# Kernel tuning notes

Hardware: AMD Instinct MI355X
Metric: run time of the kernel (lower is better)

Reference implementation:

```python
import jax, jax.numpy as jnp
import numpy as np
from jax import lax

INSZ, HSZ, NLAYERS = 1024, 1024, 2
B, T = 32, 512
FORGET_BIAS = 1.0


def setup_inputs() -> dict:
    key = jax.random.key(0)
    ks = jax.random.split(key, 6)
    x = jax.random.normal(ks[0], (B, T, INSZ), dtype=jnp.float32)
    lengths = jax.random.randint(ks[1], (B,), 1, T + 1, dtype=jnp.int32)
    s0 = 1.0 / np.sqrt(INSZ + HSZ)
    s1 = 1.0 / np.sqrt(HSZ + HSZ)
    W0 = jax.random.uniform(ks[2], (INSZ + HSZ, 4 * HSZ), jnp.float32, -s0, s0)
    b0 = jnp.zeros((4 * HSZ,), jnp.float32)
    W1 = jax.random.uniform(ks[3], (HSZ + HSZ, 4 * HSZ), jnp.float32, -s1, s1)
    b1 = jnp.zeros((4 * HSZ,), jnp.float32)
    return {"x": x, "lengths": lengths, "W0": W0, "b0": b0, "W1": W1, "b1": b1}


def _lstm_layer(x, lengths, W, b):
    # x: [B, T, D_in]; TF LSTMCell gate order (i, j, f, o), forget_bias added to f.
    bsz = x.shape[0]
    hsz = b.shape[0] // 4
    tsteps = jnp.arange(x.shape[1])

    def step(carry, inp):
        h, c = carry
        xt, t = inp
        z = jnp.concatenate([xt, h], axis=-1) @ W + b  # [B, 4H]
        i, j, f, o = jnp.split(z, 4, axis=-1)
        c_new = jax.nn.sigmoid(f + FORGET_BIAS) * c + jax.nn.sigmoid(i) * jnp.tanh(j)
        h_new = jax.nn.sigmoid(o) * jnp.tanh(c_new)
        mask = (t < lengths)[:, None]
        # dynamic_rnn: zero outputs past sequence_length, freeze state
        h_out = jnp.where(mask, h_new, 0.0)
        h_keep = jnp.where(mask, h_new, h)
        c_keep = jnp.where(mask, c_new, c)
        return (h_keep, c_keep), h_out

    init = (jnp.zeros((bsz, hsz), x.dtype), jnp.zeros((bsz, hsz), x.dtype))
    (h_fin, c_fin), ys = lax.scan(step, init, (jnp.swapaxes(x, 0, 1), tsteps))
    return jnp.swapaxes(ys, 0, 1), h_fin, c_fin


def reference(x, lengths, W0, b0, W1, b1):
    out0, _, _ = _lstm_layer(x, lengths, W0, b0)
    out1, h1, c1 = _lstm_layer(out0, lengths, W1, b1)
    return out1, (h1, c1)
```

## Files before the change

kernel.cpp:

```cpp
#include <hip/hip_runtime.h>
#include <hip/hip_bf16.h>

typedef unsigned short u16;
typedef unsigned int u32;
typedef unsigned long long u64;
typedef short s8v __attribute__((ext_vector_type(8)));
typedef float f4v __attribute__((ext_vector_type(4)));

#define BQ 32
#define TQ 512
#define DQ 1024
#define CHUNK 128
#define NCHUNK (TQ / CHUNK)
#define NTHR 256
#define NBLK_R 256
#define NGRP 16
#define NSUB (NBLK_R / NGRP)

__device__ __host__ inline u16 f2bf(float f) {
    union { float f; unsigned u; } v; v.f = f;
    unsigned r = v.u + 0x7fffu + ((v.u >> 16) & 1u);
    return (u16)(r >> 16);
}
__device__ __host__ inline float bf2f(u16 u) {
    union { unsigned u; float f; } v; v.u = ((unsigned)u) << 16;
    return v.f;
}

__global__ void init_kernel(u32* __restrict__ zero32, size_t nzero) {
    size_t i = (size_t)blockIdx.x * blockDim.x + threadIdx.x;
    size_t stride = (size_t)gridDim.x * blockDim.x;
    for (size_t idx = i; idx < nzero; idx += stride) zero32[idx] = 0;
}

__device__ inline void unpack_pk(uint4 A, uint4 B, s8v& hi, s8v& lo) {
    union { u32 u[4]; s8v v; } H, L;
    H.u[0] = (A.x >> 16) | (A.y & 0xffff0000u); L.u[0] = (A.x & 0xffffu) | (A.y << 16);
    H.u[1] = (A.z >> 16) | (A.w & 0xffff0000u); L.u[1] = (A.z & 0xffffu) | (A.w << 16);
    H.u[2] = (B.x >> 16) | (B.y & 0xffff0000u); L.u[2] = (B.x & 0xffffu) | (B.y << 16);
    H.u[3] = (B.z >> 16) | (B.w & 0xffff0000u); L.u[3] = (B.z & 0xffffu) | (B.w << 16);
    hi = H.v; lo = L.v;
}

__global__ __launch_bounds__(NTHR) void xproj_gemm_kernel(
    const float* __restrict__ in_f32,
    const u32* __restrict__ in_pk,
    const float* __restrict__ W,
    const float* __restrict__ bias,
    float* __restrict__ zx,
    int t0)
{
    __shared__ u16 As[2][128][40];
    __shared__ u16 Bs[2][128][40];

    const int tid = threadIdx.x;
    const int bm = blockIdx.x & 31;
    const int bn = blockIdx.x >> 5;

    const int wv = tid >> 6;
    const int wm = wv >> 1, wn = wv & 1;
    const int lane = tid & 63;
    const int frow = lane & 15;
    const int quad = lane >> 4;

    const int am = tid >> 1;
    const int akh = (tid & 1) * 16;
    const int amg = bm * 128 + am;
    const int ab = amg >> 7;
    const int atl = amg & 127;
    const size_t arow = ((size_t)ab * TQ + t0 + atl) * DQ;

    const int bk = tid >> 3;
    const int bng = (tid & 7) * 16;

    f4v acc[4][4];
    #pragma unroll
    for (int i = 0; i < 4; ++i)
        #pragma unroll
        for (int j = 0; j < 4; ++j) acc[i][j] = (f4v){0.f, 0.f, 0.f, 0.f};

    for (int kt = 0; kt < 32; ++kt) {
        const int k0 = kt * 32;
        if (in_f32) {
            const float* src = in_f32 + arow + k0 + akh;
            #pragma unroll
            for (int j4 = 0; j4 < 4; ++j4) {
                float4 v = ((const float4*)src)[j4];
                float vv[4] = {v.x, v.y, v.z, v.w};
                #pragma unroll
                for (int e = 0; e < 4; ++e) {
                    u16 hh = f2bf(vv[e]);
                    As[0][am][akh + j4 * 4 + e] = hh;
                    As[1][am][akh + j4 * 4 + e] = f2bf(vv[e] - bf2f(hh));
                }
            }
        } else {
            const u32* src = in_pk + arow + k0 + akh;
            #pragma unroll
            for (int j4 = 0; j4 < 4; ++j4) {
                uint4 v = ((const uint4*)src)[j4];
                u32 vv[4] = {v.x, v.y, v.z, v.w};
                #pragma unroll
                for (int e = 0; e < 4; ++e) {
                    As[0][am][akh + j4 * 4 + e] = (u16)(vv[e] >> 16);
                    As[1][am][akh + j4 * 4 + e] = (u16)(vv[e] & 0xffffu);
                }
            }
        }
        {
            const float* wsrc = W + (size_t)(k0 + bk) * (4 * DQ) + bn * 128 + bng;
            #pragma unroll
            for (int j4 = 0; j4 < 4; ++j4) {
                float4 v = ((const float4*)wsrc)[j4];
                float vv[4] = {v.x, v.y, v.z, v.w};
                #pragma unroll
                for (int e = 0; e < 4; ++e) {
                    u16 hh = f2bf(vv[e]);
                    int n = bng + j4 * 4 + e;
                    Bs[0][n][bk] = hh;
                    Bs[1][n][bk] = f2bf(vv[e] - bf2f(hh));
                }
            }
        }
        __syncthreads();

        s8v ah[4], al[4], bh[4], bl[4];
        #pragma unroll
        for (int mt = 0; mt < 4; ++mt) {
            ah[mt] = *(const s8v*)&As[0][wm * 64 + mt * 16 + frow][quad * 8];
            al[mt] = *(const s8v*)&As[1][wm * 64 + mt * 16 + frow][quad * 8];
        }
        #pragma unroll
        for (int nt = 0; nt < 4; ++nt) {
            bh[nt] = *(const s8v*)&Bs[0][wn * 64 + nt * 16 + frow][quad * 8];
            bl[nt] = *(const s8v*)&Bs[1][wn * 64 + nt * 16 + frow][quad * 8];
        }
        #pragma unroll
        for (int mt = 0; mt < 4; ++mt)
            #pragma unroll
            for (int nt = 0; nt < 4; ++nt) {
                acc[mt][nt] = __builtin_amdgcn_mfma_f32_16x16x32_bf16(ah[mt], bh[nt], acc[mt][nt], 0, 0, 0);
                acc[mt][nt] = __builtin_amdgcn_mfma_f32_16x16x32_bf16(al[mt], bh[nt], acc[mt][nt], 0, 0, 0);
                acc[mt][nt] = __builtin_amdgcn_mfma_f32_16x16x32_bf16(ah[mt], bl[nt], acc[mt][nt], 0, 0, 0);
            }
        __syncthreads();
    }

    float bv[4];
    #pragma unroll
    for (int nt = 0; nt < 4; ++nt) bv[nt] = bias[bn * 128 + wn * 64 + nt * 16 + frow];
    #pragma unroll
    for (int mt = 0; mt < 4; ++mt) {
        #pragma unroll
        for (int nt = 0; nt < 4; ++nt) {
            int col = bn * 128 + wn * 64 + nt * 16 + frow;
            #pragma unroll
            for (int r = 0; r < 4; ++r) {
                int row = bm * 128 + wm * 64 + mt * 16 + quad * 4 + r;
                zx[(size_t)row * (4 * DQ) + col] = acc[mt][nt][r] + bv[nt];
            }
        }
    }
}

__global__ __launch_bounds__(NTHR, 1) void lstm_rec_kernel(
    const float* __restrict__ zx,
    const float* __restrict__ W,
    const int* __restrict__ lens,
    u32* __restrict__ h32,
    u32* __restrict__ subc,
    u32* __restrict__ topc,
    float* __restrict__ state_h,
    float* __restrict__ state_c,
    u32* __restrict__ out_pk,
    float* __restrict__ out_f32,
    float* __restrict__ hc_out,
    int t0, int is_last)
{
    __shared__ u16 wt[2][32][1032];
    __shared__ float red[4][16][36];

    const int tid = threadIdx.x;
    const int blk = blockIdx.x;
    const int bg = blk & 1;
    const int cg = blk >> 1;
    const int grp = blk & (NGRP - 1);

    for (int idx = tid; idx < 32 * 1024; idx += NTHR) {
        int n = idx & 31, k = idx >> 5;
        int c = n >> 2, g = n & 3;
        float w = W[(size_t)(DQ + k) * (4 * DQ) + g * DQ + cg * 8 + c];
        u16 wh = f2bf(w);
        wt[0][n][k] = wh;
        wt[1][n][k] = f2bf(w - bf2f(wh));
    }

    const int gb_l = tid >> 3;
    const int gc = tid & 7;
    const int b_g = bg * 16 + gb_l;
    const int hcol = cg * 8 + gc;
    float c_state = 0.f, h_state = 0.f;
    int mylen = 0;
    if (tid < 128) {
        mylen = lens[b_g];
        h_state = state_h[(size_t)b_g * DQ + hcol];
        c_state = state_c[(size_t)b_g * DQ + hcol];
    }

    const int wave = tid >> 6;
    const int lane = tid & 63;
    const int frow = lane & 15;
    const int quad = lane >> 4;
    const int ksrc = wave * 256;
    const u32* hrow = h32 + (size_t)(bg * 16 + frow) * DQ + ksrc + quad * 8;

    __syncthreads();

    const int tend = t0 + CHUNK;
    for (int t = t0; t < tend; ++t) {
        const u32* hp = hrow + (size_t)((t & 1) ^ 1) * (BQ * DQ);
        uint4 q[16];
        asm volatile(
            "global_load_dwordx4 %0, %16, off sc0 sc1\n\t"
            "global_load_dwordx4 %1, %16, off offset:16 sc0 sc1\n\t"
            "global_load_dwordx4 %2, %16, off offset:128 sc0 sc1\n\t"
            "global_load_dwordx4 %3, %16, off offset:144 sc0 sc1\n\t"
            "global_load_dwordx4 %4, %16, off offset:256 sc0 sc1\n\t"
            "global_load_dwordx4 %5, %16, off offset:272 sc0 sc1\n\t"
            "global_load_dwordx4 %6, %16, off offset:384 sc0 sc1\n\t"
            "global_load_dwordx4 %7, %16, off offset:400 sc0 sc1\n\t"
            "global_load_dwordx4 %8, %16, off offset:512 sc0 sc1\n\t"
            "global_load_dwordx4 %9, %16, off offset:528 sc0 sc1\n\t"
            "global_load_dwordx4 %10, %16, off offset:640 sc0 sc1\n\t"
            "global_load_dwordx4 %11, %16, off offset:656 sc0 sc1\n\t"
            "global_load_dwordx4 %12, %16, off offset:768 sc0 sc1\n\t"
            "global_load_dwordx4 %13, %16, off offset:784 sc0 sc1\n\t"
            "global_load_dwordx4 %14, %16, off offset:896 sc0 sc1\n\t"
            "global_load_dwordx4 %15, %16, off offset:912 sc0 sc1\n\t"
            "s_waitcnt vmcnt(0)"
            : "=&v"(q[0]), "=&v"(q[1]), "=&v"(q[2]), "=&v"(q[3]),
              "=&v"(q[4]), "=&v"(q[5]), "=&v"(q[6]), "=&v"(q[7]),
              "=&v"(q[8]), "=&v"(q[9]), "=&v"(q[10]), "=&v"(q[11]),
              "=&v"(q[12]), "=&v"(q[13]), "=&v"(q[14]), "=&v"(q[15])
            : "v"(hp)
            : "memory");

        f4v acc0 = {0.f, 0.f, 0.f, 0.f};
        f4v acc1 = {0.f, 0.f, 0.f, 0.f};
        #pragma unroll
        for (int s = 0; s < 8; ++s) {
            s8v a_h, a_l;
            unpack_pk(q[2 * s], q[2 * s + 1], a_h, a_l);
            const int koff = ksrc + s * 32 + quad * 8;
            s8v b0h = *(const s8v*)&wt[0][frow][koff];
            s8v b0l = *(const s8v*)&wt[1][frow][koff];
            s8v b1h = *(const s8v*)&wt[0][16 + frow][koff];
            s8v b1l = *(const s8v*)&wt[1][16 + frow][koff];
            acc0 = __builtin_amdgcn_mfma_f32_16x16x32_bf16(a_h, b0h, acc0, 0, 0, 0);
            acc1 = __builtin_amdgcn_mfma_f32_16x16x32_bf16(a_h, b1h, acc1, 0, 0, 0);
            acc0 = __builtin_amdgcn_mfma_f32_16x16x32_bf16(a_l, b0h, acc0, 0, 0, 0);
            acc1 = __builtin_amdgcn_mfma_f32_16x16x32_bf16(a_l, b1h, acc1, 0, 0, 0);
            acc0 = __builtin_amdgcn_mfma_f32_16x16x32_bf16(a_h, b0l, acc0, 0, 0, 0);
            acc1 = __builtin_amdgcn_mfma_f32_16x16x32_bf16(a_h, b1l, acc1, 0, 0, 0);
        }
        #pragma unroll
        for (int r = 0; r < 4; ++r) {
            red[wave][quad * 4 + r][frow] = acc0[r];
            red[wave][quad * 4 + r][16 + frow] = acc1[r];
        }

        float zxv[4];
        if (tid < 128) {
            size_t base = ((size_t)b_g * CHUNK + (t - t0)) * (4 * DQ) + hcol;
            #pragma unroll
            for (int g = 0; g < 4; ++g) zxv[g] = zx[base + (size_t)g * DQ];
        }
        __syncthreads();

        if (tid < 128) {
            float z[4];
            #pragma unroll
            for (int g = 0; g < 4; ++g) {
                int n = gc * 4 + g;
                z[g] = red[0][gb_l][n] + red[1][gb_l][n] + red[2][gb_l][n] + red[3][gb_l][n]
                     + zxv[g];
            }
            float si = 1.f / (1.f + __expf(-z[0]));
            float sf = 1.f / (1.f + __expf(-(z[2] + 1.0f)));
            float so = 1.f / (1.f + __expf(-z[3]));
            float cn = sf * c_state + si * tanhf(z[1]);
            float hn = so * tanhf(cn);
            bool m = (t < mylen);
            float hk = m ? hn : h_state;
            float ck = m ? cn : c_state;
            float ho = m ? hn : 0.f;
            h_state = hk; c_state = ck;

            u16 hh = f2bf(hk);
            u16 hl = f2bf(hk - bf2f(hh));
            u32 packed = ((u32)hh << 16) | (u32)hl;
            __hip_atomic_store(h32 + (size_t)(t & 1) * (BQ * DQ) + (size_t)b_g * DQ + hcol,
                               packed, __ATOMIC_RELAXED, __HIP_MEMORY_SCOPE_AGENT);

            size_t oidx = ((size_t)b_g * TQ + t) * DQ + hcol;
            if (is_last) {
                out_f32[oidx] = ho;
            } else {
                u16 oh = f2bf(ho);
                u16 ol = f2bf(ho - bf2f(oh));
                out_pk[oidx] = ((u32)oh << 16) | (u32)ol;
            }
        }

        asm volatile("s_waitcnt vmcnt(0)" ::: "memory");
        __syncthreads();
        if (t < tend - 1) {
            if (tid == 0) {
                u32 old = atomicAdd(&subc[(t * NGRP + grp) * 16], 1u);
                if (old == NSUB - 1) atomicAdd(&topc[t * 16], 1u);
                while (__hip_atomic_load(&topc[t * 16], __ATOMIC_RELAXED,
                                         __HIP_MEMORY_SCOPE_AGENT) < NGRP) { }
            }
            __syncthreads();
        }
    }

    if (tid < 128) {
        state_h[(size_t)b_g * DQ + hcol] = h_state;
        state_c[(size_t)b_g * DQ + hcol] = c_state;
        if (is_last && tend == TQ) {
            hc_out[(size_t)b_g * DQ + hcol] = h_state;
            hc_out[(size_t)BQ * DQ + (size_t)b_g * DQ + hcol] = c_state;
        }
    }
}

extern "C" void kernel_launch(void* const* d_in, const int* in_sizes, int n_in,
                              void* d_out, int out_size, void* d_ws, size_t ws_size,
                              hipStream_t stream) {
    const float* x    = (const float*)d_in[0];
    const int*   lens = (const int*)d_in[1];
    const float* W0   = (const float*)d_in[2];
    const float* b0   = (const float*)d_in[3];
    const float* W1   = (const float*)d_in[4];
    const float* b1   = (const float*)d_in[5];
    float* out = (float*)d_out;

    const size_t N = (size_t)BQ * TQ * DQ;
    const size_t ZXN = (size_t)BQ * CHUNK * 4 * DQ;
    const size_t HD = (size_t)BQ * DQ;

    float* zx   = (float*)d_ws;
    u32* o0_pk  = (u32*)(zx + ZXN);
    u32* h32_0  = o0_pk + N;
    u32* h32_1  = h32_0 + 2 * HD;
    float* sh0  = (float*)(h32_1 + 2 * HD);
    float* sc0  = sh0 + HD;
    float* sh1  = sc0 + HD;
    float* sc1  = sh1 + HD;
    u32* sub0   = (u32*)(sc1 + HD);
    u32* top0   = sub0 + (size_t)TQ * NGRP * 16;
    u32* sub1   = top0 + (size_t)TQ * 16;
    u32* top1   = sub1 + (size_t)TQ * NGRP * 16;
    u32* zend   = top1 + (size_t)TQ * 16;
    const size_t nzero = (size_t)(zend - h32_0);

    init_kernel<<<256, 256, 0, stream>>>(h32_0, nzero);

    for (int c = 0; c < NCHUNK; ++c) {
        int t0 = c * CHUNK;
        xproj_gemm_kernel<<<1024, NTHR, 0, stream>>>(x, nullptr, W0, b0, zx, t0);
        lstm_rec_kernel<<<NBLK_R, NTHR, 0, stream>>>(
            zx, W0, lens, h32_0, sub0, top0, sh0, sc0,
            o0_pk, nullptr, nullptr, t0, 0);
    }
    for (int c = 0; c < NCHUNK; ++c) {
        int t0 = c * CHUNK;
        xproj_gemm_kernel<<<1024, NTHR, 0, stream>>>(nullptr, o0_pk, W1, b1, zx, t0);
        lstm_rec_kernel<<<NBLK_R, NTHR, 0, stream>>>(
            zx, W1, lens, h32_1, sub1, top1, sh1, sc1,
            nullptr, out, out + N, t0, 1);
    }
}
```

Baseline: 8.444 ms.

## Use per-timestep hidden history buffer and split grid barrier by batch group

The recurrent kernel now writes each step's packed hidden state into a (T+1)-row history buffer. That buffer also serves as layer-0 output, so the separate out_pk store goes away, and the layer-1 input projection reads it directly and zeroes rows past each sequence length. The per-step grid barrier now counts only the 128 blocks sharing a batch half, since those blocks only read hidden rows from that half. The inline-asm cache-bypassing loads become plain vector loads, which is safe because each step reads a fresh address. In exchange, the layer-1 recurrence reuses the same buffer, so it depends on the chunk ordering to avoid overwriting inputs before they are consumed.

```diff
diff --git a/kernel.cpp b/kernel.cpp
--- a/kernel.cpp
+++ b/kernel.cpp
@@ -14,8 +14,6 @@
 #define NCHUNK (TQ / CHUNK)
 #define NTHR 256
 #define NBLK_R 256
-#define NGRP 16
-#define NSUB (NBLK_R / NGRP)
 
 __device__ __host__ inline u16 f2bf(float f) {
     union { float f; unsigned u; } v; v.f = f;
@@ -27,10 +25,12 @@
     return v.f;
 }
 
-__global__ void init_kernel(u32* __restrict__ zero32, size_t nzero) {
+__global__ void init_kernel(u32* __restrict__ z0, size_t n0,
+                            u32* __restrict__ z1, size_t n1) {
     size_t i = (size_t)blockIdx.x * blockDim.x + threadIdx.x;
     size_t stride = (size_t)gridDim.x * blockDim.x;
-    for (size_t idx = i; idx < nzero; idx += stride) zero32[idx] = 0;
+    for (size_t idx = i; idx < n0; idx += stride) z0[idx] = 0;
+    for (size_t idx = i; idx < n1; idx += stride) z1[idx] = 0;
 }
 
 __device__ inline void unpack_pk(uint4 A, uint4 B, s8v& hi, s8v& lo) {
@@ -44,7 +44,8 @@
 
 __global__ __launch_bounds__(NTHR) void xproj_gemm_kernel(
     const float* __restrict__ in_f32,
-    const u32* __restrict__ in_pk,
+    const u32* __restrict__ hh,
+    const int* __restrict__ lens,
     const float* __restrict__ W,
     const float* __restrict__ bias,
     float* __restrict__ zx,
@@ -68,10 +69,19 @@
     const int amg = bm * 128 + am;
     const int ab = amg >> 7;
     const int atl = amg & 127;
-    const size_t arow = ((size_t)ab * TQ + t0 + atl) * DQ;
+    const int at = t0 + atl;
 
     const int bk = tid >> 3;
     const int bng = (tid & 7) * 16;
+
+    bool arow_live = true;
+    size_t arow;
+    if (in_f32) {
+        arow = ((size_t)ab * TQ + at) * DQ;
+    } else {
+        arow = ((size_t)(at + 1) * BQ + ab) * DQ;
+        arow_live = (at < lens[ab]);
+    }
 
     f4v acc[4][4];
     #pragma unroll
@@ -89,16 +99,17 @@
                 float vv[4] = {v.x, v.y, v.z, v.w};
                 #pragma unroll
                 for (int e = 0; e < 4; ++e) {
-                    u16 hh = f2bf(vv[e]);
-                    As[0][am][akh + j4 * 4 + e] = hh;
-                    As[1][am][akh + j4 * 4 + e] = f2bf(vv[e] - bf2f(hh));
+                    u16 hh16 = f2bf(vv[e]);
+                    As[0][am][akh + j4 * 4 + e] = hh16;
+                    As[1][am][akh + j4 * 4 + e] = f2bf(vv[e] - bf2f(hh16));
                 }
             }
         } else {
-            const u32* src = in_pk + arow + k0 + akh;
+            const u32* src = hh + arow + k0 + akh;
             #pragma unroll
             for (int j4 = 0; j4 < 4; ++j4) {
                 uint4 v = ((const uint4*)src)[j4];
+                if (!arow_live) { v.x = v.y = v.z = v.w = 0; }
                 u32 vv[4] = {v.x, v.y, v.z, v.w};
                 #pragma unroll
                 for (int e = 0; e < 4; ++e) {
@@ -115,10 +126,10 @@
                 float vv[4] = {v.x, v.y, v.z, v.w};
                 #pragma unroll
                 for (int e = 0; e < 4; ++e) {
-                    u16 hh = f2bf(vv[e]);
+                    u16 hh16 = f2bf(vv[e]);
                     int n = bng + j4 * 4 + e;
-                    Bs[0][n][bk] = hh;
-                    Bs[1][n][bk] = f2bf(vv[e] - bf2f(hh));
+                    Bs[0][n][bk] = hh16;
+                    Bs[1][n][bk] = f2bf(vv[e] - bf2f(hh16));
                 }
             }
         }
@@ -167,12 +178,11 @@
     const float* __restrict__ zx,
     const float* __restrict__ W,
     const int* __restrict__ lens,
-    u32* __restrict__ h32,
+    u32* __restrict__ hh,
     u32* __restrict__ subc,
     u32* __restrict__ topc,
     float* __restrict__ state_h,
     float* __restrict__ state_c,
-    u32* __restrict__ out_pk,
     float* __restrict__ out_f32,
     float* __restrict__ hc_out,
     int t0, int is_last)
@@ -184,7 +194,7 @@
     const int blk = blockIdx.x;
     const int bg = blk & 1;
     const int cg = blk >> 1;
-    const int grp = blk & (NGRP - 1);
+    const int grp = (blk >> 1) & 7;
 
     for (int idx = tid; idx < 32 * 1024; idx += NTHR) {
         int n = idx & 31, k = idx >> 5;
@@ -212,38 +222,18 @@
     const int frow = lane & 15;
     const int quad = lane >> 4;
     const int ksrc = wave * 256;
-    const u32* hrow = h32 + (size_t)(bg * 16 + frow) * DQ + ksrc + quad * 8;
 
     __syncthreads();
 
     const int tend = t0 + CHUNK;
     for (int t = t0; t < tend; ++t) {
-        const u32* hp = hrow + (size_t)((t & 1) ^ 1) * (BQ * DQ);
+        const u32* hp = hh + ((size_t)t * BQ + (bg * 16 + frow)) * DQ + ksrc + quad * 8;
         uint4 q[16];
-        asm volatile(
-            "global_load_dwordx4 %0, %16, off sc0 sc1\n\t"
-            "global_load_dwordx4 %1, %16, off offset:16 sc0 sc1\n\t"
-            "global_load_dwordx4 %2, %16, off offset:128 sc0 sc1\n\t"
-            "global_load_dwordx4 %3, %16, off offset:144 sc0 sc1\n\t"
-            "global_load_dwordx4 %4, %16, off offset:256 sc0 sc1\n\t"
-            "global_load_dwordx4 %5, %16, off offset:272 sc0 sc1\n\t"
-            "global_load_dwordx4 %6, %16, off offset:384 sc0 sc1\n\t"
-            "global_load_dwordx4 %7, %16, off offset:400 sc0 sc1\n\t"
-            "global_load_dwordx4 %8, %16, off offset:512 sc0 sc1\n\t"
-            "global_load_dwordx4 %9, %16, off offset:528 sc0 sc1\n\t"
-            "global_load_dwordx4 %10, %16, off offset:640 sc0 sc1\n\t"
-            "global_load_dwordx4 %11, %16, off offset:656 sc0 sc1\n\t"
-            "global_load_dwordx4 %12, %16, off offset:768 sc0 sc1\n\t"
-            "global_load_dwordx4 %13, %16, off offset:784 sc0 sc1\n\t"
-            "global_load_dwordx4 %14, %16, off offset:896 sc0 sc1\n\t"
-            "global_load_dwordx4 %15, %16, off offset:912 sc0 sc1\n\t"
-            "s_waitcnt vmcnt(0)"
-            : "=&v"(q[0]), "=&v"(q[1]), "=&v"(q[2]), "=&v"(q[3]),
-              "=&v"(q[4]), "=&v"(q[5]), "=&v"(q[6]), "=&v"(q[7]),
-              "=&v"(q[8]), "=&v"(q[9]), "=&v"(q[10]), "=&v"(q[11]),
-              "=&v"(q[12]), "=&v"(q[13]), "=&v"(q[14]), "=&v"(q[15])
-            : "v"(hp)
-            : "memory");
+        #pragma unroll
+        for (int s = 0; s < 8; ++s) {
+            q[2 * s]     = ((const uint4*)(hp + s * 32))[0];
+            q[2 * s + 1] = ((const uint4*)(hp + s * 32))[1];
+        }
 
         f4v acc0 = {0.f, 0.f, 0.f, 0.f};
         f4v acc1 = {0.f, 0.f, 0.f, 0.f};
@@ -293,22 +283,17 @@
             bool m = (t < mylen);
             float hk = m ? hn : h_state;
             float ck = m ? cn : c_state;
-            float ho = m ? hn : 0.f;
             h_state = hk; c_state = ck;
 
-            u16 hh = f2bf(hk);
-            u16 hl = f2bf(hk - bf2f(hh));
-            u32 packed = ((u32)hh << 16) | (u32)hl;
-            __hip_atomic_store(h32 + (size_t)(t & 1) * (BQ * DQ) + (size_t)b_g * DQ + hcol,
+            u16 hh16 = f2bf(hk);
+            u16 hl16 = f2bf(hk - bf2f(hh16));
+            u32 packed = ((u32)hh16 << 16) | (u32)hl16;
+            __hip_atomic_store(hh + ((size_t)(t + 1) * BQ + b_g) * DQ + hcol,
                                packed, __ATOMIC_RELAXED, __HIP_MEMORY_SCOPE_AGENT);
 
-            size_t oidx = ((size_t)b_g * TQ + t) * DQ + hcol;
             if (is_last) {
-                out_f32[oidx] = ho;
-            } else {
-                u16 oh = f2bf(ho);
-                u16 ol = f2bf(ho - bf2f(oh));
-                out_pk[oidx] = ((u32)oh << 16) | (u32)ol;
+                float ho = m ? hn : 0.f;
+                out_f32[((size_t)b_g * TQ + t) * DQ + hcol] = ho;
             }
         }
 
@@ -316,10 +301,12 @@
         __syncthreads();
         if (t < tend - 1) {
             if (tid == 0) {
-                u32 old = atomicAdd(&subc[(t * NGRP + grp) * 16], 1u);
-                if (old == NSUB - 1) atomicAdd(&topc[t * 16], 1u);
-                while (__hip_atomic_load(&topc[t * 16], __ATOMIC_RELAXED,
-                                         __HIP_MEMORY_SCOPE_AGENT) < NGRP) { }
+                u32* sc = &subc[((t * 2 + bg) * 8 + grp) * 16];
+                u32* tc = &topc[(t * 2 + bg) * 16];
+                u32 old = atomicAdd(sc, 1u);
+                if (old == 15) atomicAdd(tc, 1u);
+                while (__hip_atomic_load(tc, __ATOMIC_RELAXED,
+                                         __HIP_MEMORY_SCOPE_AGENT) < 8) { }
             }
             __syncthreads();
         }
@@ -346,39 +333,37 @@
     const float* b1   = (const float*)d_in[5];
     float* out = (float*)d_out;
 
-    const size_t N = (size_t)BQ * TQ * DQ;
+    const size_t N   = (size_t)BQ * TQ * DQ;
     const size_t ZXN = (size_t)BQ * CHUNK * 4 * DQ;
-    const size_t HD = (size_t)BQ * DQ;
-
-    float* zx   = (float*)d_ws;
-    u32* o0_pk  = (u32*)(zx + ZXN);
-    u32* h32_0  = o0_pk + N;
-    u32* h32_1  = h32_0 + 2 * HD;
-    float* sh0  = (float*)(h32_1 + 2 * HD);
-    float* sc0  = sh0 + HD;
-    float* sh1  = sc0 + HD;
-    float* sc1  = sh1 + HD;
-    u32* sub0   = (u32*)(sc1 + HD);
-    u32* top0   = sub0 + (size_t)TQ * NGRP * 16;
-    u32* sub1   = top0 + (size_t)TQ * 16;
-    u32* top1   = sub1 + (size_t)TQ * NGRP * 16;
-    u32* zend   = top1 + (size_t)TQ * 16;
-    const size_t nzero = (size_t)(zend - h32_0);
-
-    init_kernel<<<256, 256, 0, stream>>>(h32_0, nzero);
+    const size_t HD  = (size_t)BQ * DQ;
+
+    float* zx  = (float*)d_ws;
+    u32* hh    = (u32*)(zx + ZXN);
+    float* sh0 = (float*)(hh + (size_t)(TQ + 1) * HD);
+    float* sc0 = sh0 + HD;
+    float* sh1 = sc0 + HD;
+    float* sc1 = sh1 + HD;
+    u32* sub0  = (u32*)(sc1 + HD);
+    u32* top0  = sub0 + (size_t)TQ * 2 * 8 * 16;
+    u32* sub1  = top0 + (size_t)TQ * 2 * 16;
+    u32* top1  = sub1 + (size_t)TQ * 2 * 8 * 16;
+    u32* zend  = top1 + (size_t)TQ * 2 * 16;
+    const size_t nzero = (size_t)(zend - (u32*)sh0);
+
+    init_kernel<<<256, 256, 0, stream>>>(hh, HD, (u32*)sh0, nzero);
 
     for (int c = 0; c < NCHUNK; ++c) {
         int t0 = c * CHUNK;
-        xproj_gemm_kernel<<<1024, NTHR, 0, stream>>>(x, nullptr, W0, b0, zx, t0);
+        xproj_gemm_kernel<<<1024, NTHR, 0, stream>>>(x, nullptr, lens, W0, b0, zx, t0);
         lstm_rec_kernel<<<NBLK_R, NTHR, 0, stream>>>(
-            zx, W0, lens, h32_0, sub0, top0, sh0, sc0,
-            o0_pk, nullptr, nullptr, t0, 0);
+            zx, W0, lens, hh, sub0, top0, sh0, sc0,
+            nullptr, nullptr, t0, 0);
     }
     for (int c = 0; c < NCHUNK; ++c) {
         int t0 = c * CHUNK;
-        xproj_gemm_kernel<<<1024, NTHR, 0, stream>>>(nullptr, o0_pk, W1, b1, zx, t0);
+        xproj_gemm_kernel<<<1024, NTHR, 0, stream>>>(nullptr, hh, lens, W1, b1, zx, t0);
         lstm_rec_kernel<<<NBLK_R, NTHR, 0, stream>>>(
-            zx, W1, lens, h32_1, sub1, top1, sh1, sc1,
-            nullptr, out, out + N, t0, 1);
-    }
-}
+            zx, W1, lens, hh, sub1, top1, sh1, sc1,
+            out, out + N, t0, 1);
+    }
+}
```

After: 7.437 ms. 11.9% less time.
